# Optimization experiments

Measured on AMD Instinct MI355X. Metric: run time of the kernel, lower is better.

## Reference

```python
import jax, jax.numpy as jnp
import numpy as np
from jax import lax

D_MODEL = 1024
D_STATE = 16
D_CONV = 4
D_INNER = 2 * D_MODEL
B_SZ = 2
L_SEQ = 1024
EPS = 1e-5


def setup_inputs() -> dict:
    key = jax.random.key(0)
    ks = jax.random.split(key, 8)
    s = lambda k, shape, scale: jax.random.normal(k, shape, jnp.float32) * scale
    return {
        "x": jax.random.normal(ks[0], (B_SZ, L_SEQ, D_MODEL), jnp.float32),
        "norm_w": jnp.ones((D_MODEL,), jnp.float32),
        "norm_b": jnp.zeros((D_MODEL,), jnp.float32),
        "in_proj_w": s(ks[1], (2 * D_INNER, D_MODEL), 0.02),
        "in_proj_b": jnp.zeros((2 * D_INNER,), jnp.float32),
        "conv_w": s(ks[2], (D_INNER, 1, D_CONV), 0.1),   # torch Conv1d weight (out, in/groups, k)
        "conv_b": jnp.zeros((D_INNER,), jnp.float32),
        "x_proj_w": s(ks[3], (2 * D_STATE, D_INNER), 0.02),
        "x_proj_b": jnp.zeros((2 * D_STATE,), jnp.float32),
        "dt_proj_w": s(ks[4], (D_INNER, D_INNER), 0.02),
        "dt_proj_b": jnp.zeros((D_INNER,), jnp.float32),
        "A_log": s(ks[5], (D_INNER, D_STATE), 1.0),
        "D_param": jnp.ones((D_INNER,), jnp.float32),
        "out_proj_w": s(ks[6], (D_MODEL, D_INNER), 0.02),
        "out_proj_b": jnp.zeros((D_MODEL,), jnp.float32),
    }


def _layernorm(x, w, b):
    mu = jnp.mean(x, axis=-1, keepdims=True)
    var = jnp.mean(jnp.square(x - mu), axis=-1, keepdims=True)
    return (x - mu) * lax.rsqrt(var + EPS) * w + b


def _silu(x):
    return x * jax.nn.sigmoid(x)


def _selective_scan(u, delta, A, B_ssm, C_ssm):
    # u, delta: (B, L, d_inner); A: (d_inner, d_state); B_ssm, C_ssm: (B, L, d_state)
    dA = jnp.exp(delta[..., None] * A)                    # (B, L, d_inner, d_state)
    dBu = (delta * u)[..., None] * B_ssm[:, :, None, :]   # (B, L, d_inner, d_state)
    # time-major for scan
    dA_t = jnp.moveaxis(dA, 1, 0)
    dBu_t = jnp.moveaxis(dBu, 1, 0)
    C_t = jnp.moveaxis(C_ssm, 1, 0)

    def step(h, inp):
        dA_i, dBu_i, c_i = inp
        h = dA_i * h + dBu_i                              # (B, d_inner, d_state)
        y = jnp.einsum('bds,bs->bd', h, c_i)
        return h, y

    h0 = jnp.zeros((u.shape[0], u.shape[2], A.shape[1]), u.dtype)
    _, ys = lax.scan(step, h0, (dA_t, dBu_t, C_t))
    return jnp.moveaxis(ys, 0, 1)                         # (B, L, d_inner)


def reference(x, norm_w, norm_b, in_proj_w, in_proj_b, conv_w, conv_b,
              x_proj_w, x_proj_b, dt_proj_w, dt_proj_b, A_log, D_param,
              out_proj_w, out_proj_b):
    residual = x
    xn = _layernorm(x, norm_w, norm_b)
    xz = xn @ in_proj_w.T + in_proj_b                     # (B, L, 2*d_inner)
    xc, z = jnp.split(xz, 2, axis=-1)
    # depthwise causal conv1d (torch pads both sides d_conv-1 then slices :L == left pad)
    kern = jnp.transpose(conv_w, (2, 1, 0))               # (k, 1, d_inner) for 'LIO'
    xc = lax.conv_general_dilated(
        xc, kern, window_strides=(1,), padding=[(D_CONV - 1, 0)],
        dimension_numbers=('NLC', 'LIO', 'NLC'), feature_group_count=D_INNER) + conv_b
    u = _silu(xc)
    x_db = u @ x_proj_w.T + x_proj_b                      # (B, L, 2*d_state)
    B_ssm, C_ssm = jnp.split(x_db, 2, axis=-1)
    delta = jax.nn.softplus(u @ dt_proj_w.T + dt_proj_b)  # (B, L, d_inner)
    A = -jnp.exp(A_log)
    y = _selective_scan(u, delta, A, B_ssm, C_ssm)
    y = y + u * D_param
    y = y * _silu(z)
    out = y @ out_proj_w.T + out_proj_b
    return residual + out
```

## Files before the change

### kernel.cpp

```cpp
#include <hip/hip_runtime.h>

#define DM   1024
#define DI   2048
#define LSEQ 1024
#define BSZ  2
#define MROWS (BSZ*LSEQ)
#define NCH   (BSZ*DI)
#define SCHUNK 32
#define STEPS  32
#define PLANE  (NCH*16)

typedef __attribute__((ext_vector_type(4)))  float  f32x4;
typedef __attribute__((ext_vector_type(16))) float  f32x16;
typedef __attribute__((ext_vector_type(8)))  __bf16 bf16x8;

__device__ __forceinline__ unsigned short f2bf(float f) {
  union { float f; unsigned int u; } v; v.f = f;
  unsigned int u = v.u;
  unsigned int r = (u + 0x7fffu + ((u >> 16) & 1u)) >> 16;
  return (unsigned short)r;
}

__device__ __forceinline__ void load_lds16(const void* g, void* l) {
  __builtin_amdgcn_global_load_lds((const __attribute__((address_space(1))) void*)g,
                                   (__attribute__((address_space(3))) void*)l, 16, 0, 0);
}

__global__ __launch_bounds__(256) void ln_cast(const float* __restrict__ x,
    const float* __restrict__ w, const float* __restrict__ b,
    unsigned short* __restrict__ out)
{
  int row = blockIdx.x, tid = threadIdx.x;
  const float4* xr = (const float4*)(x + (size_t)row * DM);
  float4 v = xr[tid];
  float s  = v.x + v.y + v.z + v.w;
  float s2 = v.x*v.x + v.y*v.y + v.z*v.z + v.w*v.w;
  #pragma unroll
  for (int off = 32; off > 0; off >>= 1) { s += __shfl_down(s, off); s2 += __shfl_down(s2, off); }
  __shared__ float ss[4], sq[4];
  if ((tid & 63) == 0) { ss[tid >> 6] = s; sq[tid >> 6] = s2; }
  __syncthreads();
  float mean = (ss[0]+ss[1]+ss[2]+ss[3]) * (1.0f/DM);
  float var  = (sq[0]+sq[1]+sq[2]+sq[3]) * (1.0f/DM) - mean*mean;
  float rs = rsqrtf(var + 1e-5f);
  float4 wv = ((const float4*)w)[tid];
  float4 bv = ((const float4*)b)[tid];
  ushort4 o;
  o.x = f2bf((v.x-mean)*rs*wv.x + bv.x);
  o.y = f2bf((v.y-mean)*rs*wv.y + bv.y);
  o.z = f2bf((v.z-mean)*rs*wv.z + bv.z);
  o.w = f2bf((v.w-mean)*rs*wv.w + bv.w);
  ((ushort4*)(out + (size_t)row * DM))[tid] = o;
}

__global__ __launch_bounds__(256) void castk(const float* __restrict__ in,
    unsigned short* __restrict__ out, int n4)
{
  int i = blockIdx.x * 256 + threadIdx.x;
  int stride = gridDim.x * 256;
  for (; i < n4; i += stride) {
    float4 v = ((const float4*)in)[i];
    ushort4 o;
    o.x = f2bf(v.x); o.y = f2bf(v.y); o.z = f2bf(v.z); o.w = f2bf(v.w);
    ((ushort4*)out)[i] = o;
  }
}

template<int EPI>
__global__ __launch_bounds__(256) void gemm_bt(
    const unsigned short* __restrict__ A, const unsigned short* __restrict__ Bw,
    const float* __restrict__ bias, const float* __restrict__ resid,
    float* __restrict__ C, int N, int K)
{
  __shared__ unsigned short As[2][128*32];
  __shared__ unsigned short Bs[2][64*32];
  const int tid  = threadIdx.x;
  const int lane = tid & 63;
  const int w    = tid >> 6;
  const int m0 = blockIdx.y * 128;
  const int n0 = blockIdx.x * 64;
  const int wm = w >> 1, wn = w & 1;
  const int r16 = lane & 15;
  const int kg  = lane >> 4;
  const int kg2 = kg ^ ((r16 >> 1) & 3);

  const int srow = tid >> 2;
  const int kl   = (tid & 3) ^ ((srow >> 1) & 3);
  const unsigned short* gaBase = A  + (size_t)(m0 + srow) * K + kl * 8;
  const unsigned short* gbBase = Bw + (size_t)(n0 + srow) * K + kl * 8;

  f32x4 acc[4][2] = {};

  load_lds16(gaBase,                 (char*)As[0] + tid*16);
  load_lds16(gaBase + (size_t)64*K,  (char*)As[0] + 4096 + tid*16);
  load_lds16(gbBase,                 (char*)Bs[0] + tid*16);
  __syncthreads();

  int cur = 0;
  for (int kt = 0; kt < K; kt += 32) {
    if (kt + 32 < K) {
      const unsigned short* ga = gaBase + kt + 32;
      const unsigned short* gb = gbBase + kt + 32;
      load_lds16(ga,                 (char*)As[cur^1] + tid*16);
      load_lds16(ga + (size_t)64*K,  (char*)As[cur^1] + 4096 + tid*16);
      load_lds16(gb,                 (char*)Bs[cur^1] + tid*16);
    }
    bf16x8 av[4], bv[2];
    #pragma unroll
    for (int i = 0; i < 4; ++i)
      av[i] = *(const bf16x8*)((const char*)As[cur] + (wm*64 + i*16 + r16)*64 + kg2*16);
    #pragma unroll
    for (int j = 0; j < 2; ++j)
      bv[j] = *(const bf16x8*)((const char*)Bs[cur] + (wn*32 + j*16 + r16)*64 + kg2*16);
    #pragma unroll
    for (int i = 0; i < 4; ++i)
      #pragma unroll
      for (int j = 0; j < 2; ++j)
        acc[i][j] = __builtin_amdgcn_mfma_f32_16x16x32_bf16(av[i], bv[j], acc[i][j], 0, 0, 0);
    __syncthreads();
    cur ^= 1;
  }

  #pragma unroll
  for (int i = 0; i < 4; ++i) {
    int rbase = m0 + wm*64 + i*16 + kg*4;
    #pragma unroll
    for (int j = 0; j < 2; ++j) {
      int col = n0 + wn*32 + j*16 + r16;
      float bcol = bias[col];
      #pragma unroll
      for (int r = 0; r < 4; ++r) {
        int row = rbase + r;
        float v = acc[i][j][r] + bcol;
        if (EPI == 1) v = (v > 20.f) ? v : log1pf(__expf(v));
        if (EPI == 2) v += resid[(size_t)row * N + col];
        C[(size_t)row * N + col] = v;
      }
    }
  }
}

__global__ __launch_bounds__(256) void conv_silu(const float* __restrict__ xz,
    const float* __restrict__ cw, const float* __restrict__ cb,
    float* __restrict__ u, unsigned short* __restrict__ u_bf)
{
  int idx = blockIdx.x * 256 + threadIdx.x;
  int d = idx & (DI-1);
  int m = idx >> 11;
  int l = m & (LSEQ-1);
  const float* col = xz + (size_t)m * (2*DI) + d;
  float acc = cb[d];
  float w0 = cw[d*4+0], w1 = cw[d*4+1], w2 = cw[d*4+2], w3 = cw[d*4+3];
  acc += w3 * col[0];
  if (l >= 1) acc += w2 * col[-(2*DI)];
  if (l >= 2) acc += w1 * col[-2*(2*DI)];
  if (l >= 3) acc += w0 * col[-3*(2*DI)];
  float s = acc / (1.f + __expf(-acc));
  u[idx]    = s;
  u_bf[idx] = f2bf(s);
}

__global__ __launch_bounds__(64) void xproj_mfma(const unsigned short* __restrict__ u_bf,
    const unsigned short* __restrict__ wx, const float* __restrict__ bias,
    float* __restrict__ xdb)
{
  int lane = threadIdx.x;
  int m0 = blockIdx.x * 16;
  int r16 = lane & 15, kg = lane >> 4;
  f32x4 acc0 = {}, acc1 = {};
  const unsigned short* ap  = u_bf + (size_t)(m0 + r16) * DI + kg*8;
  const unsigned short* b0p = wx   + (size_t)r16        * DI + kg*8;
  const unsigned short* b1p = wx   + (size_t)(16 + r16) * DI + kg*8;
  #pragma unroll 4
  for (int kt = 0; kt < DI; kt += 32) {
    bf16x8 a  = *(const bf16x8*)(ap  + kt);
    bf16x8 b0 = *(const bf16x8*)(b0p + kt);
    bf16x8 b1 = *(const bf16x8*)(b1p + kt);
    acc0 = __builtin_amdgcn_mfma_f32_16x16x32_bf16(a, b0, acc0, 0, 0, 0);
    acc1 = __builtin_amdgcn_mfma_f32_16x16x32_bf16(a, b1, acc1, 0, 0, 0);
  }
  #pragma unroll
  for (int r = 0; r < 4; ++r) {
    int row = m0 + kg*4 + r;
    xdb[row*32 + r16]      = acc0[r] + bias[r16];
    xdb[row*32 + 16 + r16] = acc1[r] + bias[16 + r16];
  }
}

__global__ __launch_bounds__(256) void scan_p1(const float* __restrict__ delta,
    const float* __restrict__ u, const float* __restrict__ xdb,
    const float* __restrict__ A_log, float* __restrict__ agg_a, float* __restrict__ agg_b)
{
  int tid = threadIdx.x;
  int sh  = tid & 3;
  int ch  = blockIdx.x * 64 + (tid >> 2);
  int c   = blockIdx.y;
  int b = ch >> 11, d = ch & (DI-1);
  float Ads[4];
  {
    f32x4 Ar = *(const f32x4*)(A_log + d*16 + sh*4);
    #pragma unroll
    for (int s = 0; s < 4; ++s) Ads[s] = -__expf(Ar[s]);
  }
  float a[4] = {1.f,1.f,1.f,1.f}, bb[4] = {0.f,0.f,0.f,0.f};
  int row0 = b * LSEQ + c * STEPS;
  const float* dp = delta + (size_t)row0 * DI + d;
  const float* up = u     + (size_t)row0 * DI + d;
  #pragma unroll 4
  for (int t = 0; t < STEPS; ++t) {
    float dl = dp[t*DI];
    float uu = up[t*DI];
    f32x4 Bv = *(const f32x4*)(xdb + (size_t)(row0 + t) * 32 + sh*4);
    float dlu = dl * uu;
    #pragma unroll
    for (int s = 0; s < 4; ++s) {
      float dA = __expf(dl * Ads[s]);
      bb[s] = fmaf(dA, bb[s], dlu * Bv[s]);
      a[s] *= dA;
    }
  }
  int idx = c*PLANE + ch*16 + sh*4;
  f32x4 av, bv;
  #pragma unroll
  for (int s = 0; s < 4; ++s) { av[s] = a[s]; bv[s] = bb[s]; }
  *(f32x4*)(agg_a + idx) = av;
  *(f32x4*)(agg_b + idx) = bv;
}

__global__ __launch_bounds__(256) void scan_p2(const float* __restrict__ agg_a,
    const float* __restrict__ agg_b, float* __restrict__ hinit)
{
  int idx = blockIdx.x * 256 + threadIdx.x;
  float h = 0.f;
  #pragma unroll
  for (int c = 0; c < SCHUNK; ++c) {
    hinit[c*PLANE + idx] = h;
    h = fmaf(agg_a[c*PLANE + idx], h, agg_b[c*PLANE + idx]);
  }
}

__global__ __launch_bounds__(256) void scan_p3(const float* __restrict__ delta,
    const float* __restrict__ u, const float* __restrict__ xdb,
    const float* __restrict__ A_log, const float* __restrict__ Dp,
    const float* __restrict__ xz, const float* __restrict__ hinit,
    unsigned short* __restrict__ y_bf)
{
  int tid = threadIdx.x;
  int sh  = tid & 3;
  int ch  = blockIdx.x * 64 + (tid >> 2);
  int c   = blockIdx.y;
  int b = ch >> 11, d = ch & (DI-1);
  float Ads[4];
  {
    f32x4 Ar = *(const f32x4*)(A_log + d*16 + sh*4);
    #pragma unroll
    for (int s = 0; s < 4; ++s) Ads[s] = -__expf(Ar[s]);
  }
  float h[4];
  {
    f32x4 hv = *(const f32x4*)(hinit + c*PLANE + ch*16 + sh*4);
    #pragma unroll
    for (int s = 0; s < 4; ++s) h[s] = hv[s];
  }
  float Dd = Dp[d];
  int row0 = b * LSEQ + c * STEPS;
  const float* dp = delta + (size_t)row0 * DI + d;
  const float* up = u     + (size_t)row0 * DI + d;
  const float* zp = xz    + (size_t)row0 * (2*DI) + DI + d;
  unsigned short* yp = y_bf + (size_t)row0 * DI + d;
  #pragma unroll 2
  for (int t = 0; t < STEPS; ++t) {
    float dl = dp[t*DI];
    float uu = up[t*DI];
    const float* xr = xdb + (size_t)(row0 + t) * 32 + sh*4;
    f32x4 Bv = *(const f32x4*)xr;
    f32x4 Cv = *(const f32x4*)(xr + 16);
    float dlu = dl * uu;
    float y = 0.f;
    #pragma unroll
    for (int s = 0; s < 4; ++s) {
      float dA = __expf(dl * Ads[s]);
      h[s] = fmaf(dA, h[s], dlu * Bv[s]);
      y = fmaf(h[s], Cv[s], y);
    }
    y += __shfl_xor(y, 1);
    y += __shfl_xor(y, 2);
    if (sh == 0) {
      float zz = zp[t*(2*DI)];
      float yv = y + uu * Dd;
      yv *= zz / (1.f + __expf(-zz));
      yp[t*DI] = f2bf(yv);
    }
  }
}

extern "C" void kernel_launch(void* const* d_in, const int* in_sizes, int n_in,
                              void* d_out, int out_size, void* d_ws, size_t ws_size,
                              hipStream_t stream)
{
  (void)in_sizes; (void)n_in; (void)out_size;
  const float* x      = (const float*)d_in[0];
  const float* norm_w = (const float*)d_in[1];
  const float* norm_b = (const float*)d_in[2];
  const float* in_w   = (const float*)d_in[3];
  const float* in_b   = (const float*)d_in[4];
  const float* conv_w = (const float*)d_in[5];
  const float* conv_b = (const float*)d_in[6];
  const float* xp_w   = (const float*)d_in[7];
  const float* xp_b   = (const float*)d_in[8];
  const float* dt_w   = (const float*)d_in[9];
  const float* dt_b   = (const float*)d_in[10];
  const float* A_log  = (const float*)d_in[11];
  const float* D_par  = (const float*)d_in[12];
  const float* out_w  = (const float*)d_in[13];
  const float* out_b  = (const float*)d_in[14];
  float* out = (float*)d_out;

  char* p = (char*)d_ws;
  unsigned short* xn_bf = (unsigned short*)p;  p += 2048ull*1024*2;
  unsigned short* w_in  = (unsigned short*)p;  p += 4096ull*1024*2;
  unsigned short* w_dt  = (unsigned short*)p;  p += 2048ull*2048*2;
  unsigned short* w_out = (unsigned short*)p;  p += 1024ull*2048*2;
  unsigned short* wx_bf = (unsigned short*)p;  p += 32ull*2048*2;
  float*          xz    = (float*)p;           p += 2048ull*4096*4;
  float*          u_f   = (float*)p;           p += 2048ull*2048*4;
  unsigned short* u_bf  = (unsigned short*)p;  p += 2048ull*2048*2;
  float*          xdb   = (float*)p;           p += 2048ull*32*4;
  float*          delta = (float*)p;           p += 2048ull*2048*4;
  unsigned short* y_bf  = (unsigned short*)p;  p += 2048ull*2048*2;
  if ((size_t)(p - (char*)d_ws) > ws_size) return;

  float* agg_a = (float*)w_in;
  float* agg_b = (float*)w_dt;
  float* hinit = (float*)u_bf;

  ln_cast<<<MROWS, 256, 0, stream>>>(x, norm_w, norm_b, xn_bf);
  castk<<<2048, 256, 0, stream>>>(in_w,  w_in,  4096*1024/4);
  castk<<<2048, 256, 0, stream>>>(dt_w,  w_dt,  2048*2048/4);
  castk<<<1024, 256, 0, stream>>>(out_w, w_out, 1024*2048/4);
  castk<<<64,   256, 0, stream>>>(xp_w,  wx_bf, 32*2048/4);

  gemm_bt<0><<<dim3(4096/64, MROWS/128), 256, 0, stream>>>(xn_bf, w_in, in_b, nullptr, xz, 4096, 1024);
  conv_silu<<<(MROWS*DI)/256, 256, 0, stream>>>(xz, conv_w, conv_b, u_f, u_bf);
  xproj_mfma<<<MROWS/16, 64, 0, stream>>>(u_bf, wx_bf, xp_b, xdb);
  gemm_bt<1><<<dim3(2048/64, MROWS/128), 256, 0, stream>>>(u_bf, w_dt, dt_b, nullptr, delta, 2048, 2048);

  scan_p1<<<dim3(NCH/64, SCHUNK), 256, 0, stream>>>(delta, u_f, xdb, A_log, agg_a, agg_b);
  scan_p2<<<PLANE/256, 256, 0, stream>>>(agg_a, agg_b, hinit);
  scan_p3<<<dim3(NCH/64, SCHUNK), 256, 0, stream>>>(delta, u_f, xdb, A_log, D_par, xz, hinit, y_bf);

  gemm_bt<2><<<dim3(1024/64, MROWS/128), 256, 0, stream>>>(y_bf, w_out, out_b, x, out, 1024, 2048);
}
```

Baseline: 229.7 us.

## Deepen GEMM pipeline with BK=64 tiles, prefetch-two-ahead and workgroup swizzle

The bf16 GEMM now stages 64-wide K tiles into LDS and keeps two tiles in flight, using explicit vmcnt waits and raw barriers in place of a full __syncthreads per step. The LDS XOR swizzle is widened to 8 chunks to match the 128-byte rows. Workgroup IDs are remapped so that neighbouring blocks share A/B tiles in L2. The aim is to hide global-load latency and halve the number of barriers, at the cost of twice the LDS per block, which may lower occupancy.

```diff
diff --git a/kernel.cpp b/kernel.cpp
--- a/kernel.cpp
+++ b/kernel.cpp
@@ -11,7 +11,6 @@
 #define PLANE  (NCH*16)
 
 typedef __attribute__((ext_vector_type(4)))  float  f32x4;
-typedef __attribute__((ext_vector_type(16))) float  f32x16;
 typedef __attribute__((ext_vector_type(8)))  __bf16 bf16x8;
 
 __device__ __forceinline__ unsigned short f2bf(float f) {
@@ -72,52 +71,72 @@
     const float* __restrict__ bias, const float* __restrict__ resid,
     float* __restrict__ C, int N, int K)
 {
-  __shared__ unsigned short As[2][128*32];
-  __shared__ unsigned short Bs[2][64*32];
+  __shared__ unsigned short As[2][128*64];
+  __shared__ unsigned short Bs[2][64*64];
   const int tid  = threadIdx.x;
   const int lane = tid & 63;
   const int w    = tid >> 6;
-  const int m0 = blockIdx.y * 128;
-  const int n0 = blockIdx.x * 64;
+
+  const int nbx = gridDim.x;
+  const int nwg = gridDim.x * gridDim.y;
+  int wg  = blockIdx.y * nbx + blockIdx.x;
+  int swz = (wg & 7) * (nwg >> 3) + (wg >> 3);
+  const int m0 = (swz / nbx) * 128;
+  const int n0 = (swz % nbx) * 64;
+
   const int wm = w >> 1, wn = w & 1;
   const int r16 = lane & 15;
   const int kg  = lane >> 4;
-  const int kg2 = kg ^ ((r16 >> 1) & 3);
-
-  const int srow = tid >> 2;
-  const int kl   = (tid & 3) ^ ((srow >> 1) & 3);
+
+  const int srow = tid >> 3;
+  const int kl   = (tid & 7) ^ (srow & 7);
   const unsigned short* gaBase = A  + (size_t)(m0 + srow) * K + kl * 8;
   const unsigned short* gbBase = Bw + (size_t)(n0 + srow) * K + kl * 8;
 
   f32x4 acc[4][2] = {};
 
-  load_lds16(gaBase,                 (char*)As[0] + tid*16);
-  load_lds16(gaBase + (size_t)64*K,  (char*)As[0] + 4096 + tid*16);
-  load_lds16(gbBase,                 (char*)Bs[0] + tid*16);
-  __syncthreads();
+  auto stage = [&](int buf, int kt) {
+    const unsigned short* ga = gaBase + kt;
+    load_lds16(ga,                   (char*)As[buf] + tid*16);
+    load_lds16(ga + (size_t)32*K,    (char*)As[buf] +  4096 + tid*16);
+    load_lds16(ga + (size_t)64*K,    (char*)As[buf] +  8192 + tid*16);
+    load_lds16(ga + (size_t)96*K,    (char*)As[buf] + 12288 + tid*16);
+    const unsigned short* gb = gbBase + kt;
+    load_lds16(gb,                   (char*)Bs[buf] + tid*16);
+    load_lds16(gb + (size_t)32*K,    (char*)Bs[buf] +  4096 + tid*16);
+  };
+
+  stage(0, 0);
+  stage(1, 64);
 
   int cur = 0;
-  for (int kt = 0; kt < K; kt += 32) {
-    if (kt + 32 < K) {
-      const unsigned short* ga = gaBase + kt + 32;
-      const unsigned short* gb = gbBase + kt + 32;
-      load_lds16(ga,                 (char*)As[cur^1] + tid*16);
-      load_lds16(ga + (size_t)64*K,  (char*)As[cur^1] + 4096 + tid*16);
-      load_lds16(gb,                 (char*)Bs[cur^1] + tid*16);
-    }
-    bf16x8 av[4], bv[2];
-    #pragma unroll
-    for (int i = 0; i < 4; ++i)
-      av[i] = *(const bf16x8*)((const char*)As[cur] + (wm*64 + i*16 + r16)*64 + kg2*16);
-    #pragma unroll
-    for (int j = 0; j < 2; ++j)
-      bv[j] = *(const bf16x8*)((const char*)Bs[cur] + (wn*32 + j*16 + r16)*64 + kg2*16);
-    #pragma unroll
-    for (int i = 0; i < 4; ++i)
+  for (int kt = 0; kt < K; kt += 64) {
+    if (kt + 64 < K) asm volatile("s_waitcnt vmcnt(6)" ::: "memory");
+    else             asm volatile("s_waitcnt vmcnt(0)" ::: "memory");
+    __builtin_amdgcn_s_barrier();
+
+    bf16x8 av[2][4], bv[2][2];
+    #pragma unroll
+    for (int kk = 0; kk < 2; ++kk) {
+      const int phys = (kk*4 + kg) ^ (r16 & 7);
+      #pragma unroll
+      for (int i = 0; i < 4; ++i)
+        av[kk][i] = *(const bf16x8*)((const char*)As[cur] + (wm*64 + i*16 + r16)*128 + phys*16);
       #pragma unroll
       for (int j = 0; j < 2; ++j)
-        acc[i][j] = __builtin_amdgcn_mfma_f32_16x16x32_bf16(av[i], bv[j], acc[i][j], 0, 0, 0);
-    __syncthreads();
+        bv[kk][j] = *(const bf16x8*)((const char*)Bs[cur] + (wn*32 + j*16 + r16)*128 + phys*16);
+    }
+    #pragma unroll
+    for (int kk = 0; kk < 2; ++kk)
+      #pragma unroll
+      for (int i = 0; i < 4; ++i)
+        #pragma unroll
+        for (int j = 0; j < 2; ++j)
+          acc[i][j] = __builtin_amdgcn_mfma_f32_16x16x32_bf16(av[kk][i], bv[kk][j], acc[i][j], 0, 0, 0);
+
+    asm volatile("s_waitcnt lgkmcnt(0)" ::: "memory");
+    __builtin_amdgcn_s_barrier();
+    if (kt + 128 < K) stage(cur, kt + 128);
     cur ^= 1;
   }
 
```

New measurement: 221.8 us. 1.04x faster.
